# Kernel tuning notes

Hardware: AMD Instinct MI355X
Metric: run time of the kernel (lower is better)

The kernel has to match this reference:

```python
import jax, jax.numpy as jnp
import numpy as np

LEAKY_SLOPE = 0.01  # torch nn.LeakyReLU default

def _mlp(x, w1, b1, w2, b2):
    # MLP_Layer(num_layers=2, batch_norm=False): Linear -> ReLU -> Linear
    return jax.nn.relu(x @ w1 + b1) @ w2 + b2

def _edge_softmax(scores, dst, num_nodes):
    # softmax over incoming edges of each destination node; scores: [E, H]
    m = jax.ops.segment_max(scores, dst, num_segments=num_nodes)  # [N, H]
    e = jnp.exp(scores - m[dst])
    s = jax.ops.segment_sum(e, dst, num_segments=num_nodes)       # [N, H]
    return e / s[dst]

def setup_inputs() -> dict:
    key = jax.random.key(0)
    ks = jax.random.split(key, 10)
    N, E, H = 50000, 800000, 4
    D_H, PCA, PI, HID = 64, 64, 32, 128
    inp = {
        "h":    jax.random.normal(ks[0], (N, D_H), jnp.float32),
        "pca":  jax.random.normal(ks[1], (N, PCA), jnp.float32),
        "pimg": jax.random.normal(ks[2], (N, PI), jnp.float32),
        "pca_w1": jax.random.normal(ks[3], (2 * PCA, HID), jnp.float32) * (1.0 / np.sqrt(2 * PCA)),
        "pca_b1": jnp.zeros((HID,), jnp.float32),
        "pca_w2": jax.random.normal(ks[4], (HID, H), jnp.float32) * (1.0 / np.sqrt(HID)),
        "pca_b2": jnp.zeros((H,), jnp.float32),
        "pi_w1": jax.random.normal(ks[5], (2 * PI, HID), jnp.float32) * (1.0 / np.sqrt(2 * PI)),
        "pi_b1": jnp.zeros((HID,), jnp.float32),
        "pi_w2": jax.random.normal(ks[6], (HID, H), jnp.float32) * (1.0 / np.sqrt(HID)),
        "pi_b2": jnp.zeros((H,), jnp.float32),
        "src": jax.random.randint(ks[7], (E,), 0, N, jnp.int32),
        "dst": jax.random.randint(ks[8], (E,), 0, N, jnp.int32),
    }
    return inp

def reference(h, pca, pimg, pca_w1, pca_b1, pca_w2, pca_b2,
              pi_w1, pi_b1, pi_w2, pi_b2, src, dst):
    N = h.shape[0]

    def attend(feat, w1, b1, w2, b2):
        e_feat = jnp.concatenate([feat[src], feat[dst]], axis=1)        # [E, 2F]
        score = jax.nn.leaky_relu(_mlp(e_feat, w1, b1, w2, b2), LEAKY_SLOPE)  # [E, H]
        a = _edge_softmax(score, dst, N)                                # [E, H]
        msg = h[src][:, None, :] * a[:, :, None]                        # [E, H, D]
        return jax.ops.segment_sum(msg, dst, num_segments=N)           # [N, H, D]

    out_pca = attend(pca, pca_w1, pca_b1, pca_w2, pca_b2)
    out_pi = attend(pimg, pi_w1, pi_b1, pi_w2, pi_b2)
    return jnp.concatenate([out_pca, out_pi], axis=-1)                  # [N, H, 2D]
```

## Files before the change

### kernel.cpp

```cpp
#include <hip/hip_runtime.h>
#include <hip/hip_fp16.h>

constexpr int HID = 128;
constexpr int DH  = 64;

typedef _Float16 f16x2 __attribute__((ext_vector_type(2)));
typedef _Float16 fh8   __attribute__((ext_vector_type(8)));
typedef float    f32x4v __attribute__((ext_vector_type(4)));

__device__ __forceinline__ fh8 relu8(fh8 x) {
  fh8 z = {0, 0, 0, 0, 0, 0, 0, 0};
#if __has_builtin(__builtin_elementwise_max)
  return __builtin_elementwise_max(x, z);
#else
  fh8 r;
#pragma unroll
  for (int i = 0; i < 8; i++) r[i] = x[i] > z[i] ? x[i] : z[i];
  return r;
#endif
}

__global__ void frag_setup_kernel(const float* __restrict__ w1a, const float* __restrict__ w1b,
                                  _Float16* __restrict__ fragTab) {
  int flat = blockIdx.x * 256 + threadIdx.x;
  if (flat >= 32768) return;
  int rel = flat >> 14;
  int r2 = flat & 16383;
  int g = r2 >> 10, s = (r2 >> 9) & 1, l = (r2 >> 3) & 63, j = r2 & 7;
  int bc = l & 15, bkg = l >> 4;
  int k = s * 32 + bkg * 8 + j;
  int F = rel ? 32 : 64;
  const float* w1 = rel ? w1b : w1a;
  float val = 0.f;
  if (k < F) {
    int jout = (g & 7) * 16 + bc;
    int krow = (g < 8) ? k : (F + k);
    val = w1[krow * HID + jout];
  }
  fragTab[flat] = (_Float16)val;
}

__launch_bounds__(256)
__global__ void uv_mfma_kernel(const float* __restrict__ pca, const float* __restrict__ pimg,
                               const float* __restrict__ b1a, const float* __restrict__ b1b,
                               const _Float16* __restrict__ fragTab,
                               _Float16* __restrict__ u_cat, _Float16* __restrict__ v_cat, int N) {
  __shared__ _Float16 sB[16384];
  int rel = blockIdx.y;
  const float* feat = rel ? pimg : pca;
  const float* b1   = rel ? b1b : b1a;
  int F  = rel ? 32 : 64;
  int KS = rel ? 1 : 2;
  int tid = threadIdx.x;
  {
    const fh8* srcp = (const fh8*)(fragTab + rel * 16384);
    fh8* dstp = (fh8*)sB;
    for (int i = tid; i < 2048; i += 256) dstp[i] = srcp[i];
  }
  __syncthreads();
  int lane = tid & 63, w = tid >> 6;
  int r = lane & 15, kg = lane >> 4;
  int node = blockIdx.x * 64 + w * 16 + r;
  int nclamp = node < N ? node : N - 1;
  fh8 a[2];
#pragma unroll
  for (int s = 0; s < 2; s++) {
    if (s < KS) {
      const float* fp = feat + (size_t)nclamp * F + s * 32 + kg * 8;
      float4 f0 = *(const float4*)fp;
      float4 f1 = *(const float4*)(fp + 4);
      fh8 t;
      t[0] = (_Float16)f0.x; t[1] = (_Float16)f0.y; t[2] = (_Float16)f0.z; t[3] = (_Float16)f0.w;
      t[4] = (_Float16)f1.x; t[5] = (_Float16)f1.y; t[6] = (_Float16)f1.z; t[7] = (_Float16)f1.w;
      a[s] = t;
    }
  }
  int onode0 = blockIdx.x * 64 + w * 16 + kg * 4;
  int c = lane & 15;
#pragma unroll
  for (int g = 0; g < 16; g++) {
    f32x4v acc = {0.f, 0.f, 0.f, 0.f};
    acc = __builtin_amdgcn_mfma_f32_16x16x32_f16(a[0], ((const fh8*)sB)[(g * 2 + 0) * 64 + lane], acc, 0, 0, 0);
    if (KS == 2)
      acc = __builtin_amdgcn_mfma_f32_16x16x32_f16(a[1], ((const fh8*)sB)[(g * 2 + 1) * 64 + lane], acc, 0, 0, 0);
    bool isv = g >= 8;
    int jout = (g & 7) * 16 + c;
    float bias = isv ? b1[jout] : 0.f;
    _Float16* outp = isv ? v_cat : u_cat;
    size_t colix = (size_t)rel * 128 + jout;
#pragma unroll
    for (int q = 0; q < 4; q++) {
      int on = onode0 + q;
      if (on < N) outp[(size_t)on * 256 + colix] = (_Float16)(acc[q] + bias);
    }
  }
}

__global__ void count_h16_kernel(const int* __restrict__ dst, int* __restrict__ counts, int E,
                                 const float* __restrict__ h, _Float16* __restrict__ h16, int total) {
  int i = blockIdx.x * 256 + threadIdx.x;
  if (i < E) atomicAdd(&counts[dst[i]], 1);
  int base = i * 8;
  if (base + 7 < total) {
    float4 f0 = *(const float4*)(h + base);
    float4 f1 = *(const float4*)(h + base + 4);
    fh8 t;
    t[0] = (_Float16)f0.x; t[1] = (_Float16)f0.y; t[2] = (_Float16)f0.z; t[3] = (_Float16)f0.w;
    t[4] = (_Float16)f1.x; t[5] = (_Float16)f1.y; t[6] = (_Float16)f1.z; t[7] = (_Float16)f1.w;
    *(fh8*)(h16 + base) = t;
  }
}

__launch_bounds__(256)
__global__ void scan1_kernel(const int* __restrict__ counts, int* __restrict__ bsums, int N) {
  int b = blockIdx.x, tid = threadIdx.x;
  int base = b * 1024 + tid * 4;
  int s = 0;
  if (base + 3 < N) {
    int4 v = *(const int4*)(counts + base);
    s = v.x + v.y + v.z + v.w;
  } else {
    for (int q = 0; q < 4; q++) { int idx = base + q; if (idx < N) s += counts[idx]; }
  }
#pragma unroll
  for (int o = 32; o >= 1; o >>= 1) s += __shfl_xor(s, o);
  __shared__ int ws[4];
  if ((tid & 63) == 0) ws[tid >> 6] = s;
  __syncthreads();
  if (tid == 0) bsums[b] = ws[0] + ws[1] + ws[2] + ws[3];
}

__launch_bounds__(1024)
__global__ void scan2_kernel(const int* __restrict__ bsums, int* __restrict__ bpre,
                             int* __restrict__ offsets, int NB, int N, int E) {
  int tid = threadIdx.x, lane = tid & 63, w = tid >> 6;
  int v = (tid < NB) ? bsums[tid] : 0;
  int incl = v;
#pragma unroll
  for (int o = 1; o < 64; o <<= 1) { int t = __shfl_up(incl, o); if (lane >= o) incl += t; }
  __shared__ int ws[16];
  if (lane == 63) ws[w] = incl;
  __syncthreads();
  int wpre = 0;
  for (int q = 0; q < w; q++) wpre += ws[q];
  if (tid < NB) bpre[tid] = wpre + incl - v;
  if (tid == 0) offsets[N] = E;
}

__launch_bounds__(256)
__global__ void scan3_kernel(const int* __restrict__ counts, const int* __restrict__ bpre,
                             int* __restrict__ offsets, int N) {
  int b = blockIdx.x, tid = threadIdx.x, lane = tid & 63, w = tid >> 6;
  int base = b * 1024 + tid * 4;
  int c[4] = {0, 0, 0, 0};
  if (base + 3 < N) {
    int4 v = *(const int4*)(counts + base);
    c[0] = v.x; c[1] = v.y; c[2] = v.z; c[3] = v.w;
  } else {
    for (int q = 0; q < 4; q++) { int idx = base + q; if (idx < N) c[q] = counts[idx]; }
  }
  int s = c[0] + c[1] + c[2] + c[3];
  int incl = s;
#pragma unroll
  for (int o = 1; o < 64; o <<= 1) { int t = __shfl_up(incl, o); if (lane >= o) incl += t; }
  int excl = incl - s;
  __shared__ int ws[4];
  if (lane == 63) ws[w] = incl;
  __syncthreads();
  int wpre = 0;
  for (int q = 0; q < w; q++) wpre += ws[q];
  int off = bpre[b] + wpre + excl;
  for (int q = 0; q < 4; q++) {
    int idx = base + q;
    if (idx < N) offsets[idx] = off;
    off += c[q];
  }
}

__global__ void fill_kernel(const int* __restrict__ src, const int* __restrict__ dst,
                            int* __restrict__ cursor, int2* __restrict__ edges, int E) {
  int e = blockIdx.x * 256 + threadIdx.x;
  if (e < E) {
    int d = dst[e];
    int pos = atomicAdd(&cursor[d], 1);
    edges[pos] = make_int2(src[e], d);
  }
}

__launch_bounds__(256, 8)
__global__ void score_kernel(const _Float16* __restrict__ u_cat, const _Float16* __restrict__ v_cat,
                             const int2* __restrict__ edges,
                             const float* __restrict__ w2a, const float* __restrict__ w2b,
                             const float* __restrict__ b2a, const float* __restrict__ b2b,
                             _Float16* __restrict__ ek, int E) {
  __shared__ _Float16 sB[8 * 64 * 8];
  int tid = threadIdx.x, lane = tid & 63, w = tid >> 6;
  int col = lane & 15, kg = lane >> 4;
  for (int idx = tid; idx < 4096; idx += 256) {
    int t = idx >> 9, l = (idx >> 3) & 63, j = idx & 7;
    int bc = l & 15;
    int k = t * 32 + ((l >> 4) << 3) + j;
    float val = 0.f;
    if (bc < 4) { if (k < 128) val = w2a[k * 4 + bc]; }
    else if (bc < 8) { if (k >= 128) val = w2b[(k - 128) * 4 + (bc - 4)]; }
    sB[idx] = (_Float16)val;
  }
  __syncthreads();

  int ebase = blockIdx.x * 256 + w * 64;
  const _Float16* up[4];
  const _Float16* vp[4];
#pragma unroll
  for (int m = 0; m < 4; m++) {
    int em = ebase + m * 16 + col;
    int ec = em < E ? em : 0;
    int2 sd = edges[ec];
    up[m] = u_cat + (size_t)sd.x * 256 + kg * 8;
    vp[m] = v_cat + (size_t)sd.y * 256 + kg * 8;
  }

  f32x4v acc[4];
#pragma unroll
  for (int m = 0; m < 4; m++) acc[m] = (f32x4v){0.f, 0.f, 0.f, 0.f};

#pragma unroll
  for (int t = 0; t < 8; t++) {
    fh8 bf = *(const fh8*)(sB + ((t * 64 + lane) << 3));
#pragma unroll
    for (int m = 0; m < 4; m++) {
      fh8 uu = *(const fh8*)(up[m] + t * 32);
      fh8 vv = *(const fh8*)(vp[m] + t * 32);
      acc[m] = __builtin_amdgcn_mfma_f32_16x16x32_f16(relu8(uu + vv), bf, acc[m], 0, 0, 0);
    }
  }

  if (col < 8) {
    float b2v = (col < 4) ? b2a[col] : b2b[col - 4];
#pragma unroll
    for (int m = 0; m < 4; m++) {
#pragma unroll
      for (int q = 0; q < 4; q++) {
        int er = ebase + m * 16 + kg * 4 + q;
        if (er < E) {
          float x = acc[m][q] + b2v;
          x = x > 0.f ? x : 0.01f * x;
          ek[(size_t)er * 8 + col] = (_Float16)__expf(x);
        }
      }
    }
  }
}

__launch_bounds__(256, 8)
__global__ void agg_kernel(const _Float16* __restrict__ ek, const int2* __restrict__ edges,
                           const int* __restrict__ offsets, const _Float16* __restrict__ h16,
                           float* __restrict__ out, int N) {
  int wid = blockIdx.x * 4 + (threadIdx.x >> 6);
  int lane = threadIdx.x & 63;
  if (wid >= N) return;
  int off0 = offsets[wid], off1 = offsets[wid + 1];
  int deg = off1 - off0;
  float* op = out + (size_t)wid * 512;
  if (deg == 0) {
#pragma unroll
    for (int k = 0; k < 4; k++) { op[k * 128 + lane] = 0.f; op[k * 128 + 64 + lane] = 0.f; }
    return;
  }
  float accO[8] = {0, 0, 0, 0, 0, 0, 0, 0};
  float ssum[8] = {0, 0, 0, 0, 0, 0, 0, 0};
  int last = off1 - 1;
  for (int jj = 0; jj < deg; jj += 4) {
    int i0 = off0 + jj;
    int i1 = min(i0 + 1, last), i2 = min(i0 + 2, last), i3 = min(i0 + 3, last);
    bool m1 = jj + 1 < deg, m2 = jj + 2 < deg, m3 = jj + 3 < deg;
    int s0 = edges[i0].x, s1 = edges[i1].x, s2 = edges[i2].x, s3 = edges[i3].x;
    fh8 e0 = *(const fh8*)(ek + (size_t)i0 * 8);
    fh8 e1 = *(const fh8*)(ek + (size_t)i1 * 8);
    fh8 e2 = *(const fh8*)(ek + (size_t)i2 * 8);
    fh8 e3 = *(const fh8*)(ek + (size_t)i3 * 8);
    float hv0 = (float)h16[(size_t)s0 * DH + lane];
    float hv1 = (float)h16[(size_t)s1 * DH + lane];
    float hv2 = (float)h16[(size_t)s2 * DH + lane];
    float hv3 = (float)h16[(size_t)s3 * DH + lane];
#pragma unroll
    for (int k = 0; k < 8; k++) {
      float e0v = (float)e0[k];
      float e1v = m1 ? (float)e1[k] : 0.f;
      float e2v = m2 ? (float)e2[k] : 0.f;
      float e3v = m3 ? (float)e3[k] : 0.f;
      accO[k] = fmaf(e0v, hv0, accO[k]);
      accO[k] = fmaf(e1v, hv1, accO[k]);
      accO[k] = fmaf(e2v, hv2, accO[k]);
      accO[k] = fmaf(e3v, hv3, accO[k]);
      ssum[k] += (e0v + e1v) + (e2v + e3v);
    }
  }
#pragma unroll
  for (int k = 0; k < 8; k++) {
    float rsv = 1.f / ssum[k];
    int colo = k < 4 ? k * 128 + lane : (k - 4) * 128 + 64 + lane;
    op[colo] = accO[k] * rsv;
  }
}

extern "C" void kernel_launch(void* const* d_in, const int* in_sizes, int n_in,
                              void* d_out, int out_size, void* d_ws, size_t ws_size,
                              hipStream_t stream) {
  const float* h      = (const float*)d_in[0];
  const float* pca    = (const float*)d_in[1];
  const float* pimg   = (const float*)d_in[2];
  const float* pca_w1 = (const float*)d_in[3];
  const float* pca_b1 = (const float*)d_in[4];
  const float* pca_w2 = (const float*)d_in[5];
  const float* pca_b2 = (const float*)d_in[6];
  const float* pi_w1  = (const float*)d_in[7];
  const float* pi_b1  = (const float*)d_in[8];
  const float* pi_w2  = (const float*)d_in[9];
  const float* pi_b2  = (const float*)d_in[10];
  const int*   src    = (const int*)d_in[11];
  const int*   dst    = (const int*)d_in[12];
  int N = in_sizes[0] / 64;
  int E = in_sizes[11];
  float* out = (float*)d_out;

  char* ws = (char*)d_ws;
  size_t o = 0;
  auto alloc = [&](size_t bytes) { void* p = ws + o; o += (bytes + 255) & ~(size_t)255; return p; };
  _Float16* u_cat  = (_Float16*)alloc((size_t)N * 256 * 2);
  _Float16* v_cat  = (_Float16*)alloc((size_t)N * 256 * 2);
  _Float16* h16    = (_Float16*)alloc((size_t)N * 64 * 2);
  _Float16* fragTab = (_Float16*)alloc(32768 * 2);
  int* counts  = (int*)alloc((size_t)N * 4);
  int* cursor  = (int*)alloc((size_t)N * 4);
  int* offsets = (int*)alloc((size_t)(N + 1) * 4);
  int* bsums   = (int*)alloc(1024 * 4);
  int* bpre    = (int*)alloc(1024 * 4);
  int2* edges  = (int2*)alloc((size_t)E * 8);
  _Float16* ekb = (_Float16*)alloc((size_t)E * 8 * 2);

  hipMemsetAsync(counts, 0, (size_t)N * 4, stream);

  frag_setup_kernel<<<128, 256, 0, stream>>>(pca_w1, pi_w1, fragTab);
  count_h16_kernel<<<(E + 255) / 256, 256, 0, stream>>>(dst, counts, E, h, h16, N * 64);
  dim3 uvgrid((N + 63) / 64, 2);
  uv_mfma_kernel<<<uvgrid, 256, 0, stream>>>(pca, pimg, pca_b1, pi_b1, fragTab, u_cat, v_cat, N);
  int NB = (N + 1023) / 1024;
  scan1_kernel<<<NB, 256, 0, stream>>>(counts, bsums, N);
  scan2_kernel<<<1, 1024, 0, stream>>>(bsums, bpre, offsets, NB, N, E);
  scan3_kernel<<<NB, 256, 0, stream>>>(counts, bpre, offsets, N);
  hipMemcpyAsync(cursor, offsets, (size_t)N * 4, hipMemcpyDeviceToDevice, stream);
  fill_kernel<<<(E + 255) / 256, 256, 0, stream>>>(src, dst, cursor, edges, E);
  score_kernel<<<(E + 255) / 256, 256, 0, stream>>>(u_cat, v_cat, edges,
                                                    pca_w2, pi_w2, pca_b2, pi_b2, ekb, E);
  agg_kernel<<<(N + 3) / 4, 256, 0, stream>>>(ekb, edges, offsets, h16, out, N);
}
```

Before: 290.1 us.

## Fuse frag setup into count kernel, transpose MFMA output, split agg edges across half-waves

The weight-fragment setup is merged into the count/h16 conversion kernel, removing one launch. The uv MFMA kernel swaps its A and B operands so each lane holds four consecutive output columns of a single node, allowing packed 4-half stores and float4 bias loads in place of scattered scalar stores. The aggregation kernel has each half-wave process alternate edges with two h columns per lane, then combines the halves with a cross-lane shuffle and writes float2 outputs. This aims to cut store transactions and widen gathers, at the cost of an extra shuffle reduction.

Measured after the change: 291.3 us. No clear change (+0.4%).

```diff
diff --git a/kernel.cpp b/kernel.cpp
--- a/kernel.cpp
+++ b/kernel.cpp
@@ -5,6 +5,7 @@
 constexpr int DH  = 64;
 
 typedef _Float16 f16x2 __attribute__((ext_vector_type(2)));
+typedef _Float16 fh4   __attribute__((ext_vector_type(4)));
 typedef _Float16 fh8   __attribute__((ext_vector_type(8)));
 typedef float    f32x4v __attribute__((ext_vector_type(4)));
 
@@ -20,24 +21,38 @@
 #endif
 }
 
-__global__ void frag_setup_kernel(const float* __restrict__ w1a, const float* __restrict__ w1b,
-                                  _Float16* __restrict__ fragTab) {
-  int flat = blockIdx.x * 256 + threadIdx.x;
-  if (flat >= 32768) return;
-  int rel = flat >> 14;
-  int r2 = flat & 16383;
-  int g = r2 >> 10, s = (r2 >> 9) & 1, l = (r2 >> 3) & 63, j = r2 & 7;
-  int bc = l & 15, bkg = l >> 4;
-  int k = s * 32 + bkg * 8 + j;
-  int F = rel ? 32 : 64;
-  const float* w1 = rel ? w1b : w1a;
-  float val = 0.f;
-  if (k < F) {
-    int jout = (g & 7) * 16 + bc;
-    int krow = (g < 8) ? k : (F + k);
-    val = w1[krow * HID + jout];
-  }
-  fragTab[flat] = (_Float16)val;
+__global__ void count_h16_frag_kernel(const int* __restrict__ dst, int* __restrict__ counts, int E,
+                                      const float* __restrict__ h, _Float16* __restrict__ h16, int total,
+                                      const float* __restrict__ w1a, const float* __restrict__ w1b,
+                                      _Float16* __restrict__ fragTab) {
+  int i = blockIdx.x * 256 + threadIdx.x;
+  if (blockIdx.x < 128) {
+    int flat = i;
+    int rel = flat >> 14;
+    int r2 = flat & 16383;
+    int g = r2 >> 10, s = (r2 >> 9) & 1, l = (r2 >> 3) & 63, j = r2 & 7;
+    int bc = l & 15, bkg = l >> 4;
+    int k = s * 32 + bkg * 8 + j;
+    int F = rel ? 32 : 64;
+    const float* w1 = rel ? w1b : w1a;
+    float val = 0.f;
+    if (k < F) {
+      int jslot = (g & 7) * 16 + bc;
+      int krow = (g < 8) ? k : (F + k);
+      val = w1[krow * HID + jslot];
+    }
+    fragTab[flat] = (_Float16)val;
+  }
+  if (i < E) atomicAdd(&counts[dst[i]], 1);
+  int base = i * 8;
+  if (base + 7 < total) {
+    float4 f0 = *(const float4*)(h + base);
+    float4 f1 = *(const float4*)(h + base + 4);
+    fh8 t;
+    t[0] = (_Float16)f0.x; t[1] = (_Float16)f0.y; t[2] = (_Float16)f0.z; t[3] = (_Float16)f0.w;
+    t[4] = (_Float16)f1.x; t[5] = (_Float16)f1.y; t[6] = (_Float16)f1.z; t[7] = (_Float16)f1.w;
+    *(fh8*)(h16 + base) = t;
+  }
 }
 
 __launch_bounds__(256)
@@ -59,10 +74,10 @@
   }
   __syncthreads();
   int lane = tid & 63, w = tid >> 6;
-  int r = lane & 15, kg = lane >> 4;
-  int node = blockIdx.x * 64 + w * 16 + r;
+  int c = lane & 15, kg = lane >> 4;
+  int node = blockIdx.x * 64 + w * 16 + c;
   int nclamp = node < N ? node : N - 1;
-  fh8 a[2];
+  fh8 bfeat[2];
 #pragma unroll
   for (int s = 0; s < 2; s++) {
     if (s < KS) {
@@ -72,42 +87,30 @@
       fh8 t;
       t[0] = (_Float16)f0.x; t[1] = (_Float16)f0.y; t[2] = (_Float16)f0.z; t[3] = (_Float16)f0.w;
       t[4] = (_Float16)f1.x; t[5] = (_Float16)f1.y; t[6] = (_Float16)f1.z; t[7] = (_Float16)f1.w;
-      a[s] = t;
-    }
-  }
-  int onode0 = blockIdx.x * 64 + w * 16 + kg * 4;
-  int c = lane & 15;
+      bfeat[s] = t;
+    }
+  }
+  float4 b1q[8];
+#pragma unroll
+  for (int g = 0; g < 8; g++) b1q[g] = *(const float4*)(b1 + g * 16 + kg * 4);
+
+  bool wr = node < N;
 #pragma unroll
   for (int g = 0; g < 16; g++) {
     f32x4v acc = {0.f, 0.f, 0.f, 0.f};
-    acc = __builtin_amdgcn_mfma_f32_16x16x32_f16(a[0], ((const fh8*)sB)[(g * 2 + 0) * 64 + lane], acc, 0, 0, 0);
+    acc = __builtin_amdgcn_mfma_f32_16x16x32_f16(((const fh8*)sB)[(g * 2 + 0) * 64 + lane], bfeat[0], acc, 0, 0, 0);
     if (KS == 2)
-      acc = __builtin_amdgcn_mfma_f32_16x16x32_f16(a[1], ((const fh8*)sB)[(g * 2 + 1) * 64 + lane], acc, 0, 0, 0);
+      acc = __builtin_amdgcn_mfma_f32_16x16x32_f16(((const fh8*)sB)[(g * 2 + 1) * 64 + lane], bfeat[1], acc, 0, 0, 0);
     bool isv = g >= 8;
-    int jout = (g & 7) * 16 + c;
-    float bias = isv ? b1[jout] : 0.f;
+    int jbase = (g & 7) * 16 + kg * 4;
+    float4 bias = isv ? b1q[g & 7] : make_float4(0.f, 0.f, 0.f, 0.f);
+    fh4 pk;
+    pk[0] = (_Float16)(acc[0] + bias.x);
+    pk[1] = (_Float16)(acc[1] + bias.y);
+    pk[2] = (_Float16)(acc[2] + bias.z);
+    pk[3] = (_Float16)(acc[3] + bias.w);
     _Float16* outp = isv ? v_cat : u_cat;
-    size_t colix = (size_t)rel * 128 + jout;
-#pragma unroll
-    for (int q = 0; q < 4; q++) {
-      int on = onode0 + q;
-      if (on < N) outp[(size_t)on * 256 + colix] = (_Float16)(acc[q] + bias);
-    }
-  }
-}
-
-__global__ void count_h16_kernel(const int* __restrict__ dst, int* __restrict__ counts, int E,
-                                 const float* __restrict__ h, _Float16* __restrict__ h16, int total) {
-  int i = blockIdx.x * 256 + threadIdx.x;
-  if (i < E) atomicAdd(&counts[dst[i]], 1);
-  int base = i * 8;
-  if (base + 7 < total) {
-    float4 f0 = *(const float4*)(h + base);
-    float4 f1 = *(const float4*)(h + base + 4);
-    fh8 t;
-    t[0] = (_Float16)f0.x; t[1] = (_Float16)f0.y; t[2] = (_Float16)f0.z; t[3] = (_Float16)f0.w;
-    t[4] = (_Float16)f1.x; t[5] = (_Float16)f1.y; t[6] = (_Float16)f1.z; t[7] = (_Float16)f1.w;
-    *(fh8*)(h16 + base) = t;
+    if (wr) *(fh4*)(outp + (size_t)node * 256 + rel * 128 + jbase) = pk;
   }
 }
 
@@ -266,40 +269,48 @@
     for (int k = 0; k < 4; k++) { op[k * 128 + lane] = 0.f; op[k * 128 + 64 + lane] = 0.f; }
     return;
   }
-  float accO[8] = {0, 0, 0, 0, 0, 0, 0, 0};
-  float ssum[8] = {0, 0, 0, 0, 0, 0, 0, 0};
+  int half = lane >> 5, lq = lane & 31;
+  float2 accO[8];
+  float ssum[8];
+#pragma unroll
+  for (int k = 0; k < 8; k++) { accO[k] = make_float2(0.f, 0.f); ssum[k] = 0.f; }
   int last = off1 - 1;
   for (int jj = 0; jj < deg; jj += 4) {
-    int i0 = off0 + jj;
-    int i1 = min(i0 + 1, last), i2 = min(i0 + 2, last), i3 = min(i0 + 3, last);
-    bool m1 = jj + 1 < deg, m2 = jj + 2 < deg, m3 = jj + 3 < deg;
-    int s0 = edges[i0].x, s1 = edges[i1].x, s2 = edges[i2].x, s3 = edges[i3].x;
-    fh8 e0 = *(const fh8*)(ek + (size_t)i0 * 8);
-    fh8 e1 = *(const fh8*)(ek + (size_t)i1 * 8);
-    fh8 e2 = *(const fh8*)(ek + (size_t)i2 * 8);
-    fh8 e3 = *(const fh8*)(ek + (size_t)i3 * 8);
-    float hv0 = (float)h16[(size_t)s0 * DH + lane];
-    float hv1 = (float)h16[(size_t)s1 * DH + lane];
-    float hv2 = (float)h16[(size_t)s2 * DH + lane];
-    float hv3 = (float)h16[(size_t)s3 * DH + lane];
+    int iA = off0 + jj + half;
+    int iB = off0 + jj + 2 + half;
+    bool mA = jj + half < deg, mB = jj + 2 + half < deg;
+    iA = min(iA, last); iB = min(iB, last);
+    int sA = edges[iA].x, sB2 = edges[iB].x;
+    fh8 eA = *(const fh8*)(ek + (size_t)iA * 8);
+    fh8 eB = *(const fh8*)(ek + (size_t)iB * 8);
+    f16x2 hA = *(const f16x2*)(h16 + (size_t)sA * DH + lq * 2);
+    f16x2 hB = *(const f16x2*)(h16 + (size_t)sB2 * DH + lq * 2);
+    float hA0 = (float)hA[0], hA1 = (float)hA[1];
+    float hB0 = (float)hB[0], hB1 = (float)hB[1];
 #pragma unroll
     for (int k = 0; k < 8; k++) {
-      float e0v = (float)e0[k];
-      float e1v = m1 ? (float)e1[k] : 0.f;
-      float e2v = m2 ? (float)e2[k] : 0.f;
-      float e3v = m3 ? (float)e3[k] : 0.f;
-      accO[k] = fmaf(e0v, hv0, accO[k]);
-      accO[k] = fmaf(e1v, hv1, accO[k]);
-      accO[k] = fmaf(e2v, hv2, accO[k]);
-      accO[k] = fmaf(e3v, hv3, accO[k]);
-      ssum[k] += (e0v + e1v) + (e2v + e3v);
+      float ea = mA ? (float)eA[k] : 0.f;
+      float eb = mB ? (float)eB[k] : 0.f;
+      accO[k].x = fmaf(ea, hA0, accO[k].x);
+      accO[k].x = fmaf(eb, hB0, accO[k].x);
+      accO[k].y = fmaf(ea, hA1, accO[k].y);
+      accO[k].y = fmaf(eb, hB1, accO[k].y);
+      ssum[k] += ea + eb;
     }
   }
 #pragma unroll
   for (int k = 0; k < 8; k++) {
+    accO[k].x += __shfl_xor(accO[k].x, 32);
+    accO[k].y += __shfl_xor(accO[k].y, 32);
+    ssum[k]   += __shfl_xor(ssum[k], 32);
+  }
+#pragma unroll
+  for (int t = 0; t < 4; t++) {
+    int k = half * 4 + t;
     float rsv = 1.f / ssum[k];
-    int colo = k < 4 ? k * 128 + lane : (k - 4) * 128 + 64 + lane;
-    op[colo] = accO[k] * rsv;
+    int colbase = (k < 4) ? (k * 128 + lq * 2) : ((k - 4) * 128 + 64 + lq * 2);
+    float2 v2 = make_float2(accO[k].x * rsv, accO[k].y * rsv);
+    *(float2*)(op + colbase) = v2;
   }
 }
 
@@ -340,8 +351,8 @@
 
   hipMemsetAsync(counts, 0, (size_t)N * 4, stream);
 
-  frag_setup_kernel<<<128, 256, 0, stream>>>(pca_w1, pi_w1, fragTab);
-  count_h16_kernel<<<(E + 255) / 256, 256, 0, stream>>>(dst, counts, E, h, h16, N * 64);
+  count_h16_frag_kernel<<<(E + 255) / 256, 256, 0, stream>>>(dst, counts, E, h, h16, N * 64,
+                                                             pca_w1, pi_w1, fragTab);
   dim3 uvgrid((N + 63) / 64, 2);
   uv_mfma_kernel<<<uvgrid, 256, 0, stream>>>(pca, pimg, pca_b1, pi_b1, fragTab, u_cat, v_cat, N);
   int NB = (N + 1023) / 1024;
```
